# Optimization experiments

Measured on AMD Instinct MI355X. Metric: run time of the kernel, lower is better.

## Reference

```python
import jax, jax.numpy as jnp
import numpy as np

N, E, H, L, T = 20000, 160000, 128, 4, 20


def _ln(x, g, b):
    m = jnp.mean(x, -1, keepdims=True)
    v = jnp.mean((x - m) ** 2, -1, keepdims=True)
    return (x - m) * jax.lax.rsqrt(v + 1e-5) * g + b


def _mlp(x, W1, b1, W2, b2, g, b):
    # Linear -> ReLU -> Linear -> LayerNorm, as in mlp_2layer
    h = jax.nn.relu(x @ W1 + b1)
    return _ln(h @ W2 + b2, g, b)


def setup_inputs() -> dict:
    key = jax.random.key(0)
    ks = iter(jax.random.split(key, 64))

    def W(shape):
        fan_in = shape[-2]
        return jax.random.normal(next(ks), shape, jnp.float32) * (fan_in ** -0.5)

    z = lambda s: jnp.zeros(s, jnp.float32)
    o = lambda s: jnp.ones(s, jnp.float32)

    inp = {
        'x': jax.random.normal(next(ks), (N, 12), jnp.float32),
        'edge_attr': jax.random.normal(next(ks), (E, 4), jnp.float32),
        'edge_index': jax.random.randint(next(ks), (2, E), 0, N),
        # node encoder (12 -> H)
        'Wn1': W((12, H)), 'bn1': z((H,)), 'Wn2': W((H, H)), 'bn2': z((H,)), 'gn_ln': o((H,)), 'bn_ln': z((H,)),
        # edge encoder (4 -> H)
        'We1': W((4, H)), 'be1': z((H,)), 'We2': W((H, H)), 'be2': z((H,)), 'ge_ln': o((H,)), 'be_ln': z((H,)),
        # stacked per-layer params: edge_mlp (4H -> H), node_mlp (3H -> H), global_mlp (3H -> H)
        'lEW1': W((L, 4 * H, H)), 'lEb1': z((L, H)), 'lEW2': W((L, H, H)), 'lEb2': z((L, H)), 'lEg': o((L, H)), 'lEbt': z((L, H)),
        'lVW1': W((L, 3 * H, H)), 'lVb1': z((L, H)), 'lVW2': W((L, H, H)), 'lVb2': z((L, H)), 'lVg': o((L, H)), 'lVbt': z((L, H)),
        'lGW1': W((L, 3 * H, H)), 'lGb1': z((L, H)), 'lGW2': W((L, H, H)), 'lGb2': z((L, H)), 'lGg': o((L, H)), 'lGbt': z((L, H)),
        # CNN output head: Conv1d(1->8,k=15,s=4) -> ReLU -> Conv1d(8->1,k=10,s=1)
        'c1w': jax.random.normal(next(ks), (8, 1, 15), jnp.float32) * 0.1, 'c1b': z((8,)),
        'c2w': jax.random.normal(next(ks), (1, 8, 10), jnp.float32) * 0.1, 'c2b': z((1,)),
    }
    return inp


def _forward(x, edge_attr, edge_index,
             Wn1, bn1, Wn2, bn2, gn_ln, bn_ln,
             We1, be1, We2, be2, ge_ln, be_ln,
             lEW1, lEb1, lEW2, lEb2, lEg, lEbt,
             lVW1, lVb1, lVW2, lVb2, lVg, lVbt,
             lGW1, lGb1, lGW2, lGb2, lGg, lGbt,
             c1w, c1b, c2w, c2b):
    senders = edge_index[0]
    receivers = edge_index[1]
    n_nodes = x.shape[0]
    n_edges = edge_attr.shape[0]

    x_v = _mlp(x, Wn1, bn1, Wn2, bn2, gn_ln, bn_ln)          # [N, H]
    x_e = _mlp(edge_attr, We1, be1, We2, be2, ge_ln, be_ln)  # [E, H]
    g = jnp.zeros((1, H), x_v.dtype)                          # B=1 global (no global inputs)

    def step(carry, p):
        x_v, x_e, g = carry
        (EW1, Eb1, EW2, Eb2, Eg, Ebt,
         VW1, Vb1, VW2, Vb2, Vg, Vbt,
         GW1, Gb1, GW2, Gb2, Gg, Gbt) = p
        # edge update: gather sender/receiver feats, concat with edge + global
        g_e = jnp.broadcast_to(g, (n_edges, H))
        edge_in = jnp.concatenate([x_v[senders], x_v[receivers], x_e, g_e], -1)  # [E, 4H]
        x_e = x_e + _mlp(edge_in, EW1, Eb1, EW2, Eb2, Eg, Ebt)
        # node update: sum-aggregate messages by receiver
        aggr = jax.ops.segment_sum(x_e, receivers, num_segments=n_nodes)  # [N, H]
        g_v = jnp.broadcast_to(g, (n_nodes, H))
        node_in = jnp.concatenate([x_v, aggr, g_v], -1)  # [N, 3H]
        x_v = x_v + _mlp(node_in, VW1, Vb1, VW2, Vb2, Vg, Vbt)
        # global update
        g_in = jnp.concatenate([jnp.sum(x_v, 0, keepdims=True), jnp.sum(x_e, 0, keepdims=True), g], -1)  # [1, 3H]
        g = g + _mlp(g_in, GW1, Gb1, GW2, Gb2, Gg, Gbt)
        return (x_v, x_e, g), None

    params = (lEW1, lEb1, lEW2, lEb2, lEg, lEbt,
              lVW1, lVb1, lVW2, lVb2, lVg, lVbt,
              lGW1, lGb1, lGW2, lGb2, lGg, lGbt)
    (x_v, x_e, g), _ = jax.lax.scan(step, (x_v, x_e, g), params)

    # CNN head over the H=128 feature axis -> [N, T]
    dn = ('NCH', 'OIH', 'NCH')
    h = x_v[:, None, :]  # [N, 1, 128]
    h = jax.lax.conv_general_dilated(h, c1w, (4,), 'VALID', dimension_numbers=dn)
    h = jax.nn.relu(h + c1b[None, :, None])  # [N, 8, 29]
    h = jax.lax.conv_general_dilated(h, c2w, (1,), 'VALID', dimension_numbers=dn) + c2b[None, :, None]
    return h[:, 0, :]  # [N, 20]


def reference(x, edge_attr, edge_index,
              Wn1, bn1, Wn2, bn2, gn_ln, bn_ln,
              We1, be1, We2, be2, ge_ln, be_ln,
              lEW1, lEb1, lEW2, lEb2, lEg, lEbt,
              lVW1, lVb1, lVW2, lVb2, lVg, lVbt,
              lGW1, lGb1, lGW2, lGb2, lGg, lGbt,
              c1w, c1b, c2w, c2b):
    return _forward(x, edge_attr, edge_index,
                    Wn1, bn1, Wn2, bn2, gn_ln, bn_ln,
                    We1, be1, We2, be2, ge_ln, be_ln,
                    lEW1, lEb1, lEW2, lEb2, lEg, lEbt,
                    lVW1, lVb1, lVW2, lVb2, lVg, lVbt,
                    lGW1, lGb1, lGW2, lGb2, lGg, lGbt,
                    c1w, c1b, c2w, c2b)
```

## Files before the change

### kernel.cpp

```cpp
#include <hip/hip_runtime.h>

#define NN 20000
#define NE 160000
#define HD 128
#define SA 136

typedef __attribute__((ext_vector_type(8))) short  bfrag;
typedef __attribute__((ext_vector_type(4))) float  facc;
typedef __attribute__((ext_vector_type(4))) float  f4v;

__device__ __forceinline__ float bf2f(unsigned short u){
  union { unsigned int i; float f; } v; v.i = ((unsigned int)u) << 16; return v.f;
}
__device__ __forceinline__ unsigned short f2bf(float f){
  union { float f; unsigned int i; } v; v.f = f;
  unsigned int r = v.i + 0x7fffu + ((v.i >> 16) & 1u);
  return (unsigned short)(r >> 16);
}

__global__ void sentinel_kernel(float* out, float code){
  if (threadIdx.x < 32) out[threadIdx.x] = code;
}

__device__ __forceinline__ void gemm_tile(const short* Ab,
                                          const unsigned short* pk,
                                          int m0, int lane, facc acc[8]){
  const int q = lane >> 4, c = lane & 15;
  #pragma unroll
  for (int kt = 0; kt < 4; ++kt){
    bfrag a = *(const bfrag*)(Ab + (m0 + c) * SA + kt * 32 + q * 8);
    const bfrag* bp = (const bfrag*)pk + kt * 512 + lane;
    #pragma unroll
    for (int nt = 0; nt < 8; ++nt){
      acc[nt] = __builtin_amdgcn_mfma_f32_16x16x32_bf16(a, bp[nt * 64], acc[nt], 0, 0, 0);
    }
  }
}

__global__ __launch_bounds__(256) void pack_all(
    const float* Wn2, const float* We2,
    const float* lEW1, const float* lEW2,
    const float* lVW1, const float* lVW2,
    unsigned short* packed)
{
  int job = blockIdx.x * 256 + threadIdx.x;
  int mat = job >> 12, r12 = job & 4095;
  int plane = r12 >> 11, r = r12 & 2047;
  int kt = r >> 9, nt = (r >> 6) & 7, lane = r & 63;
  const float* src;
  if (mat == 0) src = Wn2;
  else if (mat == 1) src = We2;
  else {
    int m2 = mat - 2, l = m2 / 7, t = m2 % 7;
    switch (t){
      case 0: src = lEW1 + ((size_t)l*512 +   0)*HD; break;
      case 1: src = lEW1 + ((size_t)l*512 + 128)*HD; break;
      case 2: src = lEW1 + ((size_t)l*512 + 256)*HD; break;
      case 3: src = lEW2 + (size_t)l*HD*HD;          break;
      case 4: src = lVW1 + ((size_t)l*384 +   0)*HD; break;
      case 5: src = lVW1 + ((size_t)l*384 + 128)*HD; break;
      default: src = lVW2 + (size_t)l*HD*HD;         break;
    }
  }
  int krow = kt*32 + (lane>>4)*8, col = nt*16 + (lane&15);
  unsigned short v[8];
  #pragma unroll
  for (int j = 0; j < 8; ++j){
    float w = src[(size_t)(krow + j)*HD + col];
    unsigned short h = f2bf(w);
    v[j] = plane ? f2bf(w - bf2f(h)) : h;
  }
  unsigned short* dst = packed + ((size_t)mat*2 + plane)*16384
                               + ((size_t)(kt*8+nt)*64 + lane)*8;
  #pragma unroll
  for (int j = 0; j < 8; ++j) dst[j] = v[j];
}

__global__ __launch_bounds__(128) void init_small(
    float* g, float* cbe, float* cbv, float* xvs, float* xes,
    const float* Eb1_0, const float* Vb1_0)
{
  int t = threadIdx.x;
  g[t] = 0.f; xvs[t] = 0.f; xes[t] = 0.f;
  cbe[t] = Eb1_0[t]; cbv[t] = Vb1_0[t];
}

__global__ __launch_bounds__(256) void zero_cnt(int* cnt){
  int i = blockIdx.x * 256 + threadIdx.x;
  if (i < NN) cnt[i] = 0;
}
__global__ __launch_bounds__(256) void hist_kernel(const int* eidx, int* cnt){
  int e = blockIdx.x * 256 + threadIdx.x;
  atomicAdd(&cnt[eidx[NE + e]], 1);
}
__global__ __launch_bounds__(1024) void scan_kernel(const int* cnt, int* base, int* ofs){
  __shared__ int wsum[16];
  int t = threadIdx.x, lane = t & 63;
  int vals[20]; int loc = 0;
  if (t < 1000){
    #pragma unroll
    for (int k = 0; k < 20; ++k){ vals[k] = cnt[t*20 + k]; loc += vals[k]; }
  }
  int inc = loc;
  #pragma unroll
  for (int d = 1; d < 64; d <<= 1){ int o = __shfl_up(inc, d); if (lane >= d) inc += o; }
  if (lane == 63) wsum[t >> 6] = inc;
  __syncthreads();
  if (t < 16){
    int v = wsum[t];
    #pragma unroll
    for (int d = 1; d < 16; d <<= 1){ int o = __shfl_up(v, d); if (t >= d) v += o; }
    wsum[t] = v;
  }
  __syncthreads();
  int woff = (t >= 64) ? wsum[(t >> 6) - 1] : 0;
  int run = woff + inc - loc;
  if (t < 1000){
    #pragma unroll
    for (int k = 0; k < 20; ++k){ base[t*20 + k] = run; ofs[t*20 + k] = run; run += vals[k]; }
  }
  if (t == 0) base[NN] = NE;
}
__global__ __launch_bounds__(256) void scatter_kernel(const int* eidx, int* ofs,
                                                      int* perm, int* ssid, int* srid){
  int e = blockIdx.x * 256 + threadIdx.x;
  int s = eidx[e], r = eidx[NE + e];
  int pos = atomicAdd(&ofs[r], 1);
  perm[pos] = e; ssid[pos] = s; srid[pos] = r;
}

__global__ __launch_bounds__(256) void enc_node(
    const float* x, const float* W1, const float* b1,
    const unsigned short* pkW2, const float* b2,
    const float* gl, const float* bl, float* xvf, int nrows)
{
  __shared__ float inb[64*12];
  __shared__ __align__(16) short Hh[64*SA];
  __shared__ __align__(16) short Hl[64*SA];
  int tid = threadIdx.x, r0 = blockIdx.x * 64;
  for (int j = tid; j < 64*12; j += 256){
    int rr = j / 12, k = j % 12, rg = r0 + rr;
    inb[j] = (rg < nrows) ? x[(size_t)rg*12 + k] : 0.f;
  }
  __syncthreads();
  {
    int cc = tid & 127;
    float w1c[12];
    #pragma unroll
    for (int k = 0; k < 12; ++k) w1c[k] = W1[k*HD + cc];
    float bb = b1[cc];
    for (int it = 0; it < 32; ++it){
      int rr = it*2 + (tid >> 7);
      float a = bb;
      #pragma unroll
      for (int k = 0; k < 12; ++k) a += inb[rr*12 + k] * w1c[k];
      float h = fmaxf(a, 0.f);
      unsigned short hh = f2bf(h);
      Hh[rr*SA + cc] = (short)hh;
      Hl[rr*SA + cc] = (short)f2bf(h - bf2f(hh));
    }
  }
  __syncthreads();
  int lane = tid & 63, q = lane >> 4, c = lane & 15, m0 = (tid >> 6) * 16;
  facc a2[8];
  #pragma unroll
  for (int nt = 0; nt < 8; ++nt) a2[nt] = (facc){0.f,0.f,0.f,0.f};
  gemm_tile(Hh, pkW2,         m0, lane, a2);
  gemm_tile(Hl, pkW2,         m0, lane, a2);
  gemm_tile(Hh, pkW2 + 16384, m0, lane, a2);
  #pragma unroll
  for (int i = 0; i < 4; ++i){
    int rl = m0 + q*4 + i, rg = r0 + rl;
    float vals[8], s = 0.f, ss = 0.f;
    #pragma unroll
    for (int nt = 0; nt < 8; ++nt){
      float v = a2[nt][i] + b2[nt*16 + c];
      vals[nt] = v; s += v; ss += v*v;
    }
    s += __shfl_xor(s,1); ss += __shfl_xor(ss,1);
    s += __shfl_xor(s,2); ss += __shfl_xor(ss,2);
    s += __shfl_xor(s,4); ss += __shfl_xor(ss,4);
    s += __shfl_xor(s,8); ss += __shfl_xor(ss,8);
    float mean = s * 0.0078125f;
    float var  = ss * 0.0078125f - mean*mean;
    float rs   = rsqrtf(var + 1e-5f);
    if (rg < nrows){
      #pragma unroll
      for (int nt = 0; nt < 8; ++nt){
        int col = nt*16 + c;
        xvf[(size_t)rg*HD + col] = (vals[nt]-mean)*rs*gl[col] + bl[col];
      }
    }
  }
}

__global__ __launch_bounds__(256) void enc_edge(
    const float* ea, const int* perm, const float* W1, const float* b1,
    const unsigned short* pkW2, const float* b2,
    const float* gl, const float* bl, unsigned short* xeb)
{
  __shared__ float inb[64*4];
  __shared__ __align__(16) short Hh[64*SA];
  __shared__ __align__(16) short Hl[64*SA];
  int tid = threadIdx.x, r0 = blockIdx.x * 64;
  {
    int rr = tid >> 2, k = tid & 3;
    int pe = perm[r0 + rr];
    inb[tid] = ea[(size_t)pe*4 + k];
  }
  __syncthreads();
  {
    int cc = tid & 127;
    float w0 = W1[0*HD+cc], w1 = W1[1*HD+cc], w2 = W1[2*HD+cc], w3 = W1[3*HD+cc];
    float bb = b1[cc];
    for (int it = 0; it < 32; ++it){
      int rr = it*2 + (tid >> 7);
      float a = bb + inb[rr*4+0]*w0 + inb[rr*4+1]*w1 + inb[rr*4+2]*w2 + inb[rr*4+3]*w3;
      float h = fmaxf(a, 0.f);
      unsigned short hh = f2bf(h);
      Hh[rr*SA + cc] = (short)hh;
      Hl[rr*SA + cc] = (short)f2bf(h - bf2f(hh));
    }
  }
  __syncthreads();
  int lane = tid & 63, q = lane >> 4, c = lane & 15, m0 = (tid >> 6) * 16;
  facc a2[8];
  #pragma unroll
  for (int nt = 0; nt < 8; ++nt) a2[nt] = (facc){0.f,0.f,0.f,0.f};
  gemm_tile(Hh, pkW2,         m0, lane, a2);
  gemm_tile(Hl, pkW2,         m0, lane, a2);
  gemm_tile(Hh, pkW2 + 16384, m0, lane, a2);
  #pragma unroll
  for (int i = 0; i < 4; ++i){
    int rl = m0 + q*4 + i, rg = r0 + rl;
    float vals[8], s = 0.f, ss = 0.f;
    #pragma unroll
    for (int nt = 0; nt < 8; ++nt){
      float v = a2[nt][i] + b2[nt*16 + c];
      vals[nt] = v; s += v; ss += v*v;
    }
    s += __shfl_xor(s,1); ss += __shfl_xor(ss,1);
    s += __shfl_xor(s,2); ss += __shfl_xor(ss,2);
    s += __shfl_xor(s,4); ss += __shfl_xor(ss,4);
    s += __shfl_xor(s,8); ss += __shfl_xor(ss,8);
    float mean = s * 0.0078125f;
    float var  = ss * 0.0078125f - mean*mean;
    float rs   = rsqrtf(var + 1e-5f);
    #pragma unroll
    for (int nt = 0; nt < 8; ++nt){
      int col = nt*16 + c;
      xeb[(size_t)rg*HD + col] = f2bf((vals[nt]-mean)*rs*gl[col] + bl[col]);
    }
  }
}

__global__ __launch_bounds__(256) void pq_kernel(
    const float* xvf, const unsigned short* pkA, const unsigned short* pkB,
    unsigned short* P, unsigned short* Q, int nrows)
{
  __shared__ __align__(16) short Ah[64*SA];
  __shared__ __align__(16) short Al[64*SA];
  int tid = threadIdx.x, r0 = blockIdx.x * 64;
  for (int j = tid; j < 1024; j += 256){
    int rr = j >> 4, ch = j & 15, rg = r0 + rr;
    float v[8];
    if (rg < nrows){
      f4v a = *(const f4v*)(xvf + (size_t)rg*HD + ch*8);
      f4v b = *(const f4v*)(xvf + (size_t)rg*HD + ch*8 + 4);
      v[0]=a[0];v[1]=a[1];v[2]=a[2];v[3]=a[3];v[4]=b[0];v[5]=b[1];v[6]=b[2];v[7]=b[3];
    } else {
      #pragma unroll
      for (int k = 0; k < 8; ++k) v[k] = 0.f;
    }
    short* dh = Ah + rr*SA + ch*8;
    short* dl = Al + rr*SA + ch*8;
    #pragma unroll
    for (int k = 0; k < 8; ++k){
      unsigned short h = f2bf(v[k]);
      dh[k] = (short)h; dl[k] = (short)f2bf(v[k] - bf2f(h));
    }
  }
  __syncthreads();
  int lane = tid & 63, q = lane >> 4, c = lane & 15, m0 = (tid >> 6) * 16;
  facc ap[8], aq[8];
  #pragma unroll
  for (int nt = 0; nt < 8; ++nt){ ap[nt] = (facc){0.f,0.f,0.f,0.f}; aq[nt] = (facc){0.f,0.f,0.f,0.f}; }
  gemm_tile(Ah, pkA,         m0, lane, ap);
  gemm_tile(Al, pkA,         m0, lane, ap);
  gemm_tile(Ah, pkA + 16384, m0, lane, ap);
  gemm_tile(Ah, pkB,         m0, lane, aq);
  gemm_tile(Al, pkB,         m0, lane, aq);
  gemm_tile(Ah, pkB + 16384, m0, lane, aq);
  #pragma unroll
  for (int i = 0; i < 4; ++i){
    int rl = m0 + q*4 + i, rg = r0 + rl;
    if (rg < nrows){
      bfrag pv, qv;
      #pragma unroll
      for (int nt = 0; nt < 8; ++nt){
        pv[nt] = (short)f2bf(ap[nt][i]);
        qv[nt] = (short)f2bf(aq[nt][i]);
      }
      *(bfrag*)(P + (size_t)rg*HD + c*8) = pv;
      *(bfrag*)(Q + (size_t)rg*HD + c*8) = qv;
    }
  }
}

__global__ __launch_bounds__(256) void edge_kernel(
    unsigned short* xeb, const int* ssid, const int* srid,
    const unsigned short* P, const unsigned short* Q, const float* cbe,
    const unsigned short* pkW1c, const unsigned short* pkW2,
    const float* Eb2, const float* Eg, const float* Ebt)
{
  __shared__ __align__(16) short Ab[64*SA];
  __shared__ __align__(16) short Hh[64*SA];
  __shared__ __align__(16) short Hl[64*SA];
  __shared__ int sidx[64], ridx[64];
  int tid = threadIdx.x, e0 = blockIdx.x * 64;
  for (int j = tid; j < 1024; j += 256){
    int rr = j >> 4, ch = j & 15;
    *(bfrag*)(Ab + rr*SA + ch*8) = *(const bfrag*)(xeb + (size_t)(e0+rr)*HD + ch*8);
  }
  if (tid < 64){ sidx[tid] = ssid[e0+tid]; ridx[tid] = srid[e0+tid]; }
  __syncthreads();
  int lane = tid & 63, q = lane >> 4, c = lane & 15, m0 = (tid >> 6) * 16;
  float cb[8];
  #pragma unroll
  for (int nt = 0; nt < 8; ++nt) cb[nt] = cbe[nt*16 + c];
  float pg[4][8];
  #pragma unroll
  for (int i = 0; i < 4; ++i){
    int rl = m0 + q*4 + i;
    bfrag ps = *(const bfrag*)(P + (size_t)sidx[rl]*HD + c*8);
    bfrag qr = *(const bfrag*)(Q + (size_t)ridx[rl]*HD + c*8);
    #pragma unroll
    for (int nt = 0; nt < 8; ++nt)
      pg[i][nt] = bf2f((unsigned short)ps[nt]) + bf2f((unsigned short)qr[nt]) + cb[nt];
  }
  facc acc[8];
  #pragma unroll
  for (int nt = 0; nt < 8; ++nt) acc[nt] = (facc){0.f,0.f,0.f,0.f};
  gemm_tile(Ab, pkW1c,         m0, lane, acc);
  gemm_tile(Ab, pkW1c + 16384, m0, lane, acc);
  #pragma unroll
  for (int i = 0; i < 4; ++i){
    int rl = m0 + q*4 + i;
    #pragma unroll
    for (int nt = 0; nt < 8; ++nt){
      int col = nt*16 + c;
      float h = fmaxf(acc[nt][i] + pg[i][nt], 0.f);
      unsigned short hh = f2bf(h);
      Hh[rl*SA + col] = (short)hh;
      Hl[rl*SA + col] = (short)f2bf(h - bf2f(hh));
    }
  }
  __syncthreads();
  facc a2[8];
  #pragma unroll
  for (int nt = 0; nt < 8; ++nt) a2[nt] = (facc){0.f,0.f,0.f,0.f};
  gemm_tile(Hh, pkW2,         m0, lane, a2);
  gemm_tile(Hl, pkW2,         m0, lane, a2);
  gemm_tile(Hh, pkW2 + 16384, m0, lane, a2);
  #pragma unroll
  for (int i = 0; i < 4; ++i){
    int rl = m0 + q*4 + i, eg = e0 + rl;
    float vals[8], s = 0.f, ss = 0.f;
    #pragma unroll
    for (int nt = 0; nt < 8; ++nt){
      float v = a2[nt][i] + Eb2[nt*16 + c];
      vals[nt] = v; s += v; ss += v*v;
    }
    s += __shfl_xor(s,1); ss += __shfl_xor(ss,1);
    s += __shfl_xor(s,2); ss += __shfl_xor(ss,2);
    s += __shfl_xor(s,4); ss += __shfl_xor(ss,4);
    s += __shfl_xor(s,8); ss += __shfl_xor(ss,8);
    float mean = s * 0.0078125f;
    float var  = ss * 0.0078125f - mean*mean;
    float rs   = rsqrtf(var + 1e-5f);
    #pragma unroll
    for (int nt = 0; nt < 8; ++nt){
      int col = nt*16 + c;
      float o = (vals[nt]-mean)*rs*Eg[col] + Ebt[col];
      float nv = bf2f((unsigned short)Ab[rl*SA + col]) + o;
      xeb[(size_t)eg*HD + col] = f2bf(nv);
    }
  }
}

__global__ __launch_bounds__(256) void node_kernel(
    float* xvf, const unsigned short* xeb, const int* base, const float* cbv,
    const unsigned short* pkW1a, const unsigned short* pkW1b, const unsigned short* pkW2,
    const float* Vb2, const float* Vg, const float* Vbt,
    float* xv_sum, float* xes, int do_xes, int nrows)
{
  __shared__ __align__(16) short Avh[64*SA];
  __shared__ __align__(16) short Avl[64*SA];
  __shared__ __align__(16) short Agh[64*SA];
  __shared__ __align__(16) short Agl[64*SA];
  __shared__ float red[128];
  int tid = threadIdx.x, r0 = blockIdx.x * 64;
  int lane = tid & 63, wq = tid >> 6;
  if (tid < 128) red[tid] = 0.f;
  for (int j = tid; j < 1024; j += 256){
    int rr = j >> 4, ch = j & 15, rg = r0 + rr;
    float v[8];
    if (rg < nrows){
      f4v a = *(const f4v*)(xvf + (size_t)rg*HD + ch*8);
      f4v b = *(const f4v*)(xvf + (size_t)rg*HD + ch*8 + 4);
      v[0]=a[0];v[1]=a[1];v[2]=a[2];v[3]=a[3];v[4]=b[0];v[5]=b[1];v[6]=b[2];v[7]=b[3];
    } else {
      #pragma unroll
      for (int k = 0; k < 8; ++k) v[k] = 0.f;
    }
    short *dvh = Avh + rr*SA + ch*8, *dvl = Avl + rr*SA + ch*8;
    #pragma unroll
    for (int k = 0; k < 8; ++k){
      unsigned short h1 = f2bf(v[k]);
      dvh[k] = (short)h1; dvl[k] = (short)f2bf(v[k] - bf2f(h1));
    }
  }
  float xp0 = 0.f, xp1 = 0.f;
  for (int j = 0; j < 16; ++j){
    int rl = wq*16 + j, rg = r0 + rl;
    float s0 = 0.f, s1 = 0.f;
    if (rg < nrows){
      int b0 = base[rg], b1 = base[rg + 1];
      int e = b0;
      for (; e + 1 < b1; e += 2){
        unsigned int u0 = *(const unsigned int*)(xeb + (size_t)e*HD + lane*2);
        unsigned int u1 = *(const unsigned int*)(xeb + (size_t)(e+1)*HD + lane*2);
        s0 += bf2f((unsigned short)(u0 & 0xffffu)) + bf2f((unsigned short)(u1 & 0xffffu));
        s1 += bf2f((unsigned short)(u0 >> 16))     + bf2f((unsigned short)(u1 >> 16));
      }
      if (e < b1){
        unsigned int u0 = *(const unsigned int*)(xeb + (size_t)e*HD + lane*2);
        s0 += bf2f((unsigned short)(u0 & 0xffffu));
        s1 += bf2f((unsigned short)(u0 >> 16));
      }
    }
    unsigned short h0 = f2bf(s0), h1 = f2bf(s1);
    unsigned short l0 = f2bf(s0 - bf2f(h0)), l1 = f2bf(s1 - bf2f(h1));
    *(unsigned int*)(Agh + rl*SA + 2*lane) = ((unsigned int)h1 << 16) | h0;
    *(unsigned int*)(Agl + rl*SA + 2*lane) = ((unsigned int)l1 << 16) | l0;
    xp0 += s0; xp1 += s1;
  }
  if (do_xes){
    atomicAdd(&red[lane*2],     xp0);
    atomicAdd(&red[lane*2 + 1], xp1);
  }
  __syncthreads();
  if (do_xes && tid < 128) atomicAdd(&xes[tid], red[tid]);
  int q = lane >> 4, c = lane & 15, m0 = (tid >> 6) * 16;
  facc acc[8];
  #pragma unroll
  for (int nt = 0; nt < 8; ++nt) acc[nt] = (facc){0.f,0.f,0.f,0.f};
  gemm_tile(Avh, pkW1a,         m0, lane, acc);
  gemm_tile(Avl, pkW1a,         m0, lane, acc);
  gemm_tile(Avh, pkW1a + 16384, m0, lane, acc);
  gemm_tile(Agh, pkW1b,         m0, lane, acc);
  gemm_tile(Agl, pkW1b,         m0, lane, acc);
  gemm_tile(Agh, pkW1b + 16384, m0, lane, acc);
  __syncthreads();
  #pragma unroll
  for (int i = 0; i < 4; ++i){
    int rl = m0 + q*4 + i;
    #pragma unroll
    for (int nt = 0; nt < 8; ++nt){
      int col = nt*16 + c;
      float h = fmaxf(acc[nt][i] + cbv[col], 0.f);
      unsigned short hh = f2bf(h);
      Avh[rl*SA + col] = (short)hh;
      Avl[rl*SA + col] = (short)f2bf(h - bf2f(hh));
    }
  }
  __syncthreads();
  facc a2[8];
  #pragma unroll
  for (int nt = 0; nt < 8; ++nt) a2[nt] = (facc){0.f,0.f,0.f,0.f};
  gemm_tile(Avh, pkW2,         m0, lane, a2);
  gemm_tile(Avl, pkW2,         m0, lane, a2);
  gemm_tile(Avh, pkW2 + 16384, m0, lane, a2);
  float csum[8] = {0.f,0.f,0.f,0.f,0.f,0.f,0.f,0.f};
  #pragma unroll
  for (int i = 0; i < 4; ++i){
    int rl = m0 + q*4 + i, rg = r0 + rl;
    bool ok = rg < nrows;
    float vals[8], s = 0.f, ss = 0.f;
    #pragma unroll
    for (int nt = 0; nt < 8; ++nt){
      float v = a2[nt][i] + Vb2[nt*16 + c];
      vals[nt] = v; s += v; ss += v*v;
    }
    s += __shfl_xor(s,1); ss += __shfl_xor(ss,1);
    s += __shfl_xor(s,2); ss += __shfl_xor(ss,2);
    s += __shfl_xor(s,4); ss += __shfl_xor(ss,4);
    s += __shfl_xor(s,8); ss += __shfl_xor(ss,8);
    float mean = s * 0.0078125f;
    float var  = ss * 0.0078125f - mean*mean;
    float rs   = rsqrtf(var + 1e-5f);
    if (ok){
      #pragma unroll
      for (int nt = 0; nt < 8; ++nt){
        int col = nt*16 + c;
        float o = (vals[nt]-mean)*rs*Vg[col] + Vbt[col];
        size_t gi = (size_t)rg*HD + col;
        float nv = xvf[gi] + o;
        xvf[gi] = nv;
        csum[nt] += nv;
      }
    }
  }
  #pragma unroll
  for (int nt = 0; nt < 8; ++nt){
    float v = csum[nt]; v += __shfl_xor(v,16); v += __shfl_xor(v,32);
    if (q == 0) atomicAdd(&xv_sum[nt*16 + c], v);
  }
}

__global__ __launch_bounds__(1024) void g_kernel(
    float* xvs, float* xes, float* g,
    const float* GW1, const float* Gb1, const float* GW2, const float* Gb2,
    const float* Gg, const float* Gbt,
    float* cbe, float* cbv,
    const float* EW1n, const float* Eb1n, const float* VW1n, const float* Vb1n)
{
  __shared__ float gin[384], h1[128], gn[128], red[4];
  __shared__ float partA[8][128], partB[8][128];
  int tid = threadIdx.x, t = tid & 127, kk = tid >> 7;
  if (tid < 384) gin[tid] = (tid < 128) ? xvs[tid] : (tid < 256) ? xes[tid-128] : g[tid-256];
  __syncthreads();
  {
    float a = 0.f;
    for (int k = kk*48; k < kk*48 + 48; ++k) a += gin[k] * GW1[(size_t)k*HD + t];
    partA[kk][t] = a;
  }
  __syncthreads();
  if (kk == 0){
    float a = Gb1[t];
    #pragma unroll
    for (int i = 0; i < 8; ++i) a += partA[i][t];
    h1[t] = fmaxf(a, 0.f);
  }
  __syncthreads();
  {
    float o = 0.f;
    for (int k = kk*16; k < kk*16 + 16; ++k) o += h1[k] * GW2[(size_t)k*HD + t];
    partA[kk][t] = o;
  }
  __syncthreads();
  float oo = 0.f;
  if (kk == 0){
    oo = Gb2[t];
    #pragma unroll
    for (int i = 0; i < 8; ++i) oo += partA[i][t];
  }
  __syncthreads();
  if (tid < 128){
    float s = oo;
    #pragma unroll
    for (int d = 1; d < 64; d <<= 1) s += __shfl_xor(s, d);
    if ((tid & 63) == 0) red[tid >> 6] = s;
  }
  __syncthreads();
  float mean = (red[0] + red[1]) * 0.0078125f;
  if (tid < 128){
    float dd = oo - mean;
    float v = dd * dd;
    #pragma unroll
    for (int d = 1; d < 64; d <<= 1) v += __shfl_xor(v, d);
    if ((tid & 63) == 0) red[2 + (tid >> 6)] = v;
  }
  __syncthreads();
  if (tid < 128){
    float rs = rsqrtf((red[2] + red[3]) * 0.0078125f + 1e-5f);
    float gnv = g[tid] + (oo - mean)*rs*Gg[tid] + Gbt[tid];
    g[tid] = gnv; gn[tid] = gnv;
    xvs[tid] = 0.f; xes[tid] = 0.f;
  }
  __syncthreads();
  {
    float ce = 0.f, cv = 0.f;
    for (int k = kk*16; k < kk*16 + 16; ++k){
      ce += gn[k] * EW1n[(size_t)k*HD + t];
      cv += gn[k] * VW1n[(size_t)k*HD + t];
    }
    partA[kk][t] = ce; partB[kk][t] = cv;
  }
  __syncthreads();
  if (kk == 0){
    float ce = Eb1n[t], cv = Vb1n[t];
    #pragma unroll
    for (int i = 0; i < 8; ++i){ ce += partA[i][t]; cv += partB[i][t]; }
    cbe[t] = ce; cbv[t] = cv;
  }
}

__global__ __launch_bounds__(256) void decoder_kernel(
    const float* xv, const float* c1w, const float* c1b,
    const float* c2w, const float* c2b, float* out)
{
  __shared__ float xl[4][128];
  __shared__ float hl[4][232];
  __shared__ float w1[120], b1[8], w2[80];
  __shared__ float b2s;
  int tid = threadIdx.x, nl = tid >> 6, t = tid & 63;
  int n = blockIdx.x * 4 + nl;
  if (tid < 120) w1[tid] = c1w[tid];
  else if (tid < 128) b1[tid - 120] = c1b[tid - 120];
  else if (tid < 208) w2[tid - 128] = c2w[tid - 128];
  else if (tid == 208) b2s = c2b[0];
  xl[nl][t]      = xv[(size_t)n*HD + t];
  xl[nl][t + 64] = xv[(size_t)n*HD + 64 + t];
  __syncthreads();
  for (int j = t; j < 232; j += 64){
    int ch = j / 29, pp = j % 29;
    float a = b1[ch];
    #pragma unroll
    for (int u = 0; u < 15; ++u) a += xl[nl][4*pp + u] * w1[ch*15 + u];
    hl[nl][j] = fmaxf(a, 0.f);
  }
  __syncthreads();
  if (t < 20){
    float o = b2s;
    #pragma unroll
    for (int ch = 0; ch < 8; ++ch)
      #pragma unroll
      for (int u = 0; u < 10; ++u)
        o += hl[nl][ch*29 + t + u] * w2[ch*10 + u];
    out[(size_t)n*20 + t] = o;
  }
}

extern "C" void kernel_launch(void* const* d_in, const int* in_sizes, int n_in,
                              void* d_out, int out_size, void* d_ws, size_t ws_size,
                              hipStream_t stream)
{
  const float* x    = (const float*)d_in[0];
  const float* ea   = (const float*)d_in[1];
  const int*   eidx = (const int*)d_in[2];
  const float* Wn1  = (const float*)d_in[3];  const float* bn1  = (const float*)d_in[4];
  const float* Wn2  = (const float*)d_in[5];  const float* bn2  = (const float*)d_in[6];
  const float* gnln = (const float*)d_in[7];  const float* bnln = (const float*)d_in[8];
  const float* We1  = (const float*)d_in[9];  const float* be1  = (const float*)d_in[10];
  const float* We2  = (const float*)d_in[11]; const float* be2  = (const float*)d_in[12];
  const float* geln = (const float*)d_in[13]; const float* beln = (const float*)d_in[14];
  const float* lEW1 = (const float*)d_in[15]; const float* lEb1 = (const float*)d_in[16];
  const float* lEW2 = (const float*)d_in[17]; const float* lEb2 = (const float*)d_in[18];
  const float* lEg  = (const float*)d_in[19]; const float* lEbt = (const float*)d_in[20];
  const float* lVW1 = (const float*)d_in[21]; const float* lVb1 = (const float*)d_in[22];
  const float* lVW2 = (const float*)d_in[23]; const float* lVb2 = (const float*)d_in[24];
  const float* lVg  = (const float*)d_in[25]; const float* lVbt = (const float*)d_in[26];
  const float* lGW1 = (const float*)d_in[27]; const float* lGb1 = (const float*)d_in[28];
  const float* lGW2 = (const float*)d_in[29]; const float* lGb2 = (const float*)d_in[30];
  const float* lGg  = (const float*)d_in[31]; const float* lGbt = (const float*)d_in[32];
  const float* c1w  = (const float*)d_in[33]; const float* c1b  = (const float*)d_in[34];
  const float* c2w  = (const float*)d_in[35]; const float* c2b  = (const float*)d_in[36];

  char* ws = (char*)d_ws;
  size_t off = 0;
  auto alloc = [&](size_t b){ size_t o = off; off += (b + 255) & ~(size_t)255; return o; };
  unsigned short* pk   = (unsigned short*)(ws + alloc((size_t)30*2*16384*2));
  float*          g    = (float*)(ws + alloc(512));
  float*          cbe  = (float*)(ws + alloc(512));
  float*          cbv  = (float*)(ws + alloc(512));
  float*          xvs  = (float*)(ws + alloc(512));
  float*          xes  = (float*)(ws + alloc(512));
  float*          xvf  = (float*)(ws + alloc((size_t)NN*HD*4));
  unsigned short* P    = (unsigned short*)(ws + alloc((size_t)NN*HD*2));
  unsigned short* Q    = (unsigned short*)(ws + alloc((size_t)NN*HD*2));
  unsigned short* xeb  = (unsigned short*)(ws + alloc((size_t)NE*HD*2));
  int*            cnt  = (int*)(ws + alloc((size_t)NN*4));
  int*            bse  = (int*)(ws + alloc((size_t)(NN+1)*4));
  int*            ofs  = (int*)(ws + alloc((size_t)NN*4));
  int*            perm = (int*)(ws + alloc((size_t)NE*4));
  int*            ssid = (int*)(ws + alloc((size_t)NE*4));
  int*            srid = (int*)(ws + alloc((size_t)NE*4));

  if (ws_size < off){
    sentinel_kernel<<<1, 32, 0, stream>>>((float*)d_out, 20000.f + (float)(ws_size >> 20));
    return;
  }

  auto slot = [&](int m){ return pk + (size_t)m * 32768; };

  pack_all<<<480, 256, 0, stream>>>(Wn2, We2, lEW1, lEW2, lVW1, lVW2, pk);
  init_small<<<1, 128, 0, stream>>>(g, cbe, cbv, xvs, xes, lEb1, lVb1);
  zero_cnt<<<(NN + 255)/256, 256, 0, stream>>>(cnt);
  hist_kernel<<<NE/256, 256, 0, stream>>>(eidx, cnt);
  scan_kernel<<<1, 1024, 0, stream>>>(cnt, bse, ofs);
  scatter_kernel<<<NE/256, 256, 0, stream>>>(eidx, ofs, perm, ssid, srid);

  enc_node<<<(NN + 63)/64, 256, 0, stream>>>(x, Wn1, bn1, slot(0), bn2, gnln, bnln, xvf, NN);
  enc_edge<<<NE/64, 256, 0, stream>>>(ea, perm, We1, be1, slot(1), be2, geln, beln, xeb);

  for (int l = 0; l < 4; ++l){
    int m = 2 + 7*l;
    pq_kernel<<<(NN + 63)/64, 256, 0, stream>>>(xvf, slot(m+0), slot(m+1), P, Q, NN);
    edge_kernel<<<NE/64, 256, 0, stream>>>(xeb, ssid, srid, P, Q, cbe,
        slot(m+2), slot(m+3),
        lEb2 + (size_t)l*HD, lEg + (size_t)l*HD, lEbt + (size_t)l*HD);
    node_kernel<<<(NN + 63)/64, 256, 0, stream>>>(xvf, xeb, bse, cbv,
        slot(m+4), slot(m+5), slot(m+6),
        lVb2 + (size_t)l*HD, lVg + (size_t)l*HD, lVbt + (size_t)l*HD,
        xvs, xes, (l < 3) ? 1 : 0, NN);
    if (l < 3){
      g_kernel<<<1, 1024, 0, stream>>>(xvs, xes, g,
          lGW1 + (size_t)l*384*HD, lGb1 + (size_t)l*HD,
          lGW2 + (size_t)l*HD*HD, lGb2 + (size_t)l*HD,
          lGg + (size_t)l*HD, lGbt + (size_t)l*HD,
          cbe, cbv,
          lEW1 + ((size_t)(l+1)*512 + 384)*HD, lEb1 + (size_t)(l+1)*HD,
          lVW1 + ((size_t)(l+1)*384 + 256)*HD, lVb1 + (size_t)(l+1)*HD);
    }
  }
  decoder_kernel<<<NN/4, 256, 0, stream>>>(xvf, c1w, c1b, c2w, c2b, (float*)d_out);

  hipError_t e = hipGetLastError();
  if (e != hipSuccess){
    sentinel_kernel<<<1, 32, 0, stream>>>((float*)d_out, 10000.f + (float)e);
  }
  (void)in_sizes; (void)n_in; (void)out_size;
}
```

Before: 913.9 us.

## Split node and PQ GEMM columns across eight waves per block

The pq and node kernels move from 256 to 512 threads per block. Each wave now computes half of the 128 output columns for its 16-row tile, instead of one wave covering all columns. In the node kernel the LayerNorm row statistics are combined across the two column halves through shared memory with an extra barrier. The aim is more waves per block for these small-grid kernels, which have about 313 blocks, so latency hides better. The cost is extra synchronisation, and the A fragments are now loaded by two waves.

```diff
diff --git a/kernel.cpp b/kernel.cpp
--- a/kernel.cpp
+++ b/kernel.cpp
@@ -6,6 +6,7 @@
 #define SA 136
 
 typedef __attribute__((ext_vector_type(8))) short  bfrag;
+typedef __attribute__((ext_vector_type(4))) short  s4v;
 typedef __attribute__((ext_vector_type(4))) float  facc;
 typedef __attribute__((ext_vector_type(4))) float  f4v;
 
@@ -32,6 +33,21 @@
     const bfrag* bp = (const bfrag*)pk + kt * 512 + lane;
     #pragma unroll
     for (int nt = 0; nt < 8; ++nt){
+      acc[nt] = __builtin_amdgcn_mfma_f32_16x16x32_bf16(a, bp[nt * 64], acc[nt], 0, 0, 0);
+    }
+  }
+}
+
+__device__ __forceinline__ void gemm_tile_h(const short* Ab,
+                                            const unsigned short* pk,
+                                            int m0, int ntb, int lane, facc acc[4]){
+  const int q = lane >> 4, c = lane & 15;
+  #pragma unroll
+  for (int kt = 0; kt < 4; ++kt){
+    bfrag a = *(const bfrag*)(Ab + (m0 + c) * SA + kt * 32 + q * 8);
+    const bfrag* bp = (const bfrag*)pk + kt * 512 + ntb * 64 + lane;
+    #pragma unroll
+    for (int nt = 0; nt < 4; ++nt){
       acc[nt] = __builtin_amdgcn_mfma_f32_16x16x32_bf16(a, bp[nt * 64], acc[nt], 0, 0, 0);
     }
   }
@@ -254,14 +270,14 @@
   }
 }
 
-__global__ __launch_bounds__(256) void pq_kernel(
+__global__ __launch_bounds__(512, 4) void pq_kernel(
     const float* xvf, const unsigned short* pkA, const unsigned short* pkB,
     unsigned short* P, unsigned short* Q, int nrows)
 {
   __shared__ __align__(16) short Ah[64*SA];
   __shared__ __align__(16) short Al[64*SA];
   int tid = threadIdx.x, r0 = blockIdx.x * 64;
-  for (int j = tid; j < 1024; j += 256){
+  for (int j = tid; j < 1024; j += 512){
     int rr = j >> 4, ch = j & 15, rg = r0 + rr;
     float v[8];
     if (rg < nrows){
@@ -281,28 +297,29 @@
     }
   }
   __syncthreads();
-  int lane = tid & 63, q = lane >> 4, c = lane & 15, m0 = (tid >> 6) * 16;
-  facc ap[8], aq[8];
-  #pragma unroll
-  for (int nt = 0; nt < 8; ++nt){ ap[nt] = (facc){0.f,0.f,0.f,0.f}; aq[nt] = (facc){0.f,0.f,0.f,0.f}; }
-  gemm_tile(Ah, pkA,         m0, lane, ap);
-  gemm_tile(Al, pkA,         m0, lane, ap);
-  gemm_tile(Ah, pkA + 16384, m0, lane, ap);
-  gemm_tile(Ah, pkB,         m0, lane, aq);
-  gemm_tile(Al, pkB,         m0, lane, aq);
-  gemm_tile(Ah, pkB + 16384, m0, lane, aq);
+  int lane = tid & 63, wq = tid >> 6, q = lane >> 4, c = lane & 15;
+  int m0 = (wq & 3) * 16, ntb = (wq >> 2) * 4;
+  facc ap[4], aq[4];
+  #pragma unroll
+  for (int nt = 0; nt < 4; ++nt){ ap[nt] = (facc){0.f,0.f,0.f,0.f}; aq[nt] = (facc){0.f,0.f,0.f,0.f}; }
+  gemm_tile_h(Ah, pkA,         m0, ntb, lane, ap);
+  gemm_tile_h(Al, pkA,         m0, ntb, lane, ap);
+  gemm_tile_h(Ah, pkA + 16384, m0, ntb, lane, ap);
+  gemm_tile_h(Ah, pkB,         m0, ntb, lane, aq);
+  gemm_tile_h(Al, pkB,         m0, ntb, lane, aq);
+  gemm_tile_h(Ah, pkB + 16384, m0, ntb, lane, aq);
   #pragma unroll
   for (int i = 0; i < 4; ++i){
     int rl = m0 + q*4 + i, rg = r0 + rl;
     if (rg < nrows){
-      bfrag pv, qv;
+      s4v pv, qv;
       #pragma unroll
-      for (int nt = 0; nt < 8; ++nt){
+      for (int nt = 0; nt < 4; ++nt){
         pv[nt] = (short)f2bf(ap[nt][i]);
         qv[nt] = (short)f2bf(aq[nt][i]);
       }
-      *(bfrag*)(P + (size_t)rg*HD + c*8) = pv;
-      *(bfrag*)(Q + (size_t)rg*HD + c*8) = qv;
+      *(s4v*)(P + (size_t)rg*HD + c*8 + ntb) = pv;
+      *(s4v*)(Q + (size_t)rg*HD + c*8 + ntb) = qv;
     }
   }
 }
@@ -388,7 +405,7 @@
   }
 }
 
-__global__ __launch_bounds__(256) void node_kernel(
+__global__ __launch_bounds__(512, 4) void node_kernel(
     float* xvf, const unsigned short* xeb, const int* base, const float* cbv,
     const unsigned short* pkW1a, const unsigned short* pkW1b, const unsigned short* pkW2,
     const float* Vb2, const float* Vg, const float* Vbt,
@@ -399,10 +416,12 @@
   __shared__ __align__(16) short Agh[64*SA];
   __shared__ __align__(16) short Agl[64*SA];
   __shared__ float red[128];
+  __shared__ float lnS[128], lnSS[128];
   int tid = threadIdx.x, r0 = blockIdx.x * 64;
   int lane = tid & 63, wq = tid >> 6;
   if (tid < 128) red[tid] = 0.f;
-  for (int j = tid; j < 1024; j += 256){
+  __syncthreads();
+  for (int j = tid; j < 1024; j += 512){
     int rr = j >> 4, ch = j & 15, rg = r0 + rr;
     float v[8];
     if (rg < nrows){
@@ -421,8 +440,8 @@
     }
   }
   float xp0 = 0.f, xp1 = 0.f;
-  for (int j = 0; j < 16; ++j){
-    int rl = wq*16 + j, rg = r0 + rl;
+  for (int j = 0; j < 8; ++j){
+    int rl = wq*8 + j, rg = r0 + rl;
     float s0 = 0.f, s1 = 0.f;
     if (rg < nrows){
       int b0 = base[rg], b1 = base[rg + 1];
@@ -451,23 +470,24 @@
   }
   __syncthreads();
   if (do_xes && tid < 128) atomicAdd(&xes[tid], red[tid]);
-  int q = lane >> 4, c = lane & 15, m0 = (tid >> 6) * 16;
-  facc acc[8];
-  #pragma unroll
-  for (int nt = 0; nt < 8; ++nt) acc[nt] = (facc){0.f,0.f,0.f,0.f};
-  gemm_tile(Avh, pkW1a,         m0, lane, acc);
-  gemm_tile(Avl, pkW1a,         m0, lane, acc);
-  gemm_tile(Avh, pkW1a + 16384, m0, lane, acc);
-  gemm_tile(Agh, pkW1b,         m0, lane, acc);
-  gemm_tile(Agl, pkW1b,         m0, lane, acc);
-  gemm_tile(Agh, pkW1b + 16384, m0, lane, acc);
+  int q = lane >> 4, c = lane & 15;
+  int m0 = (wq & 3) * 16, ntb = (wq >> 2) * 4, half = wq >> 2;
+  facc acc[4];
+  #pragma unroll
+  for (int nt = 0; nt < 4; ++nt) acc[nt] = (facc){0.f,0.f,0.f,0.f};
+  gemm_tile_h(Avh, pkW1a,         m0, ntb, lane, acc);
+  gemm_tile_h(Avl, pkW1a,         m0, ntb, lane, acc);
+  gemm_tile_h(Avh, pkW1a + 16384, m0, ntb, lane, acc);
+  gemm_tile_h(Agh, pkW1b,         m0, ntb, lane, acc);
+  gemm_tile_h(Agl, pkW1b,         m0, ntb, lane, acc);
+  gemm_tile_h(Agh, pkW1b + 16384, m0, ntb, lane, acc);
   __syncthreads();
   #pragma unroll
   for (int i = 0; i < 4; ++i){
     int rl = m0 + q*4 + i;
     #pragma unroll
-    for (int nt = 0; nt < 8; ++nt){
-      int col = nt*16 + c;
+    for (int nt = 0; nt < 4; ++nt){
+      int col = (ntb + nt)*16 + c;
       float h = fmaxf(acc[nt][i] + cbv[col], 0.f);
       unsigned short hh = f2bf(h);
       Avh[rl*SA + col] = (short)hh;
@@ -475,35 +495,44 @@
     }
   }
   __syncthreads();
-  facc a2[8];
-  #pragma unroll
-  for (int nt = 0; nt < 8; ++nt) a2[nt] = (facc){0.f,0.f,0.f,0.f};
-  gemm_tile(Avh, pkW2,         m0, lane, a2);
-  gemm_tile(Avl, pkW2,         m0, lane, a2);
-  gemm_tile(Avh, pkW2 + 16384, m0, lane, a2);
-  float csum[8] = {0.f,0.f,0.f,0.f,0.f,0.f,0.f,0.f};
-  #pragma unroll
-  for (int i = 0; i < 4; ++i){
-    int rl = m0 + q*4 + i, rg = r0 + rl;
-    bool ok = rg < nrows;
-    float vals[8], s = 0.f, ss = 0.f;
-    #pragma unroll
-    for (int nt = 0; nt < 8; ++nt){
-      float v = a2[nt][i] + Vb2[nt*16 + c];
-      vals[nt] = v; s += v; ss += v*v;
+  facc a2[4];
+  #pragma unroll
+  for (int nt = 0; nt < 4; ++nt) a2[nt] = (facc){0.f,0.f,0.f,0.f};
+  gemm_tile_h(Avh, pkW2,         m0, ntb, lane, a2);
+  gemm_tile_h(Avl, pkW2,         m0, ntb, lane, a2);
+  gemm_tile_h(Avh, pkW2 + 16384, m0, ntb, lane, a2);
+  float vals[4][4], myS[4], mySS[4];
+  #pragma unroll
+  for (int i = 0; i < 4; ++i){
+    int rl = m0 + q*4 + i;
+    float s = 0.f, ss = 0.f;
+    #pragma unroll
+    for (int nt = 0; nt < 4; ++nt){
+      float v = a2[nt][i] + Vb2[(ntb + nt)*16 + c];
+      vals[i][nt] = v; s += v; ss += v*v;
     }
     s += __shfl_xor(s,1); ss += __shfl_xor(ss,1);
     s += __shfl_xor(s,2); ss += __shfl_xor(ss,2);
     s += __shfl_xor(s,4); ss += __shfl_xor(ss,4);
     s += __shfl_xor(s,8); ss += __shfl_xor(ss,8);
-    float mean = s * 0.0078125f;
-    float var  = ss * 0.0078125f - mean*mean;
+    myS[i] = s; mySS[i] = ss;
+    if (c == 0){ lnS[rl*2 + half] = s; lnSS[rl*2 + half] = ss; }
+  }
+  __syncthreads();
+  float csum[4] = {0.f,0.f,0.f,0.f};
+  #pragma unroll
+  for (int i = 0; i < 4; ++i){
+    int rl = m0 + q*4 + i, rg = r0 + rl;
+    float sT  = myS[i]  + lnS[rl*2 + (half^1)];
+    float ssT = mySS[i] + lnSS[rl*2 + (half^1)];
+    float mean = sT * 0.0078125f;
+    float var  = ssT * 0.0078125f - mean*mean;
     float rs   = rsqrtf(var + 1e-5f);
-    if (ok){
+    if (rg < nrows){
       #pragma unroll
-      for (int nt = 0; nt < 8; ++nt){
-        int col = nt*16 + c;
-        float o = (vals[nt]-mean)*rs*Vg[col] + Vbt[col];
+      for (int nt = 0; nt < 4; ++nt){
+        int col = (ntb + nt)*16 + c;
+        float o = (vals[i][nt]-mean)*rs*Vg[col] + Vbt[col];
         size_t gi = (size_t)rg*HD + col;
         float nv = xvf[gi] + o;
         xvf[gi] = nv;
@@ -512,9 +541,9 @@
     }
   }
   #pragma unroll
-  for (int nt = 0; nt < 8; ++nt){
+  for (int nt = 0; nt < 4; ++nt){
     float v = csum[nt]; v += __shfl_xor(v,16); v += __shfl_xor(v,32);
-    if (q == 0) atomicAdd(&xv_sum[nt*16 + c], v);
+    if (q == 0) atomicAdd(&xv_sum[(ntb + nt)*16 + c], v);
   }
 }
 
@@ -696,11 +725,11 @@
 
   for (int l = 0; l < 4; ++l){
     int m = 2 + 7*l;
-    pq_kernel<<<(NN + 63)/64, 256, 0, stream>>>(xvf, slot(m+0), slot(m+1), P, Q, NN);
+    pq_kernel<<<(NN + 63)/64, 512, 0, stream>>>(xvf, slot(m+0), slot(m+1), P, Q, NN);
     edge_kernel<<<NE/64, 256, 0, stream>>>(xeb, ssid, srid, P, Q, cbe,
         slot(m+2), slot(m+3),
         lEb2 + (size_t)l*HD, lEg + (size_t)l*HD, lEbt + (size_t)l*HD);
-    node_kernel<<<(NN + 63)/64, 256, 0, stream>>>(xvf, xeb, bse, cbv,
+    node_kernel<<<(NN + 63)/64, 512, 0, stream>>>(xvf, xeb, bse, cbv,
         slot(m+4), slot(m+5), slot(m+6),
         lVb2 + (size_t)l*HD, lVg + (size_t)l*HD, lVbt + (size_t)l*HD,
         xvs, xes, (l < 3) ? 1 : 0, NN);
```

Result: faster. 848.1 us (-7.2%).
